# Kernel optimization log

Hardware: AMD Instinct MI355X
Metric: run time of the kernel (lower is better)

The kernel has to match this reference:

```python
import math
import jax, jax.numpy as jnp
import numpy as np

# ---- static module config ----
DIM = 256
NUM_HEADS = 8
WS = (12, 12)            # window size
L = WS[0] * WS[1]        # window area = 144
META_HIDDEN = 384
LOGIT_MAX = math.log(1.0 / 0.01)  # clamp max for logit scale


def _relative_coords_log() -> np.ndarray:
    """Log-spaced pairwise relative coordinates, shape (L*L, 2)."""
    ys, xs = np.meshgrid(np.arange(WS[0]), np.arange(WS[1]), indexing="ij")
    coords = np.stack([ys.ravel(), xs.ravel()], axis=0)          # (2, L)
    rel = coords[:, :, None] - coords[:, None, :]                # (2, L, L)
    rel = rel.transpose(1, 2, 0).reshape(-1, 2).astype(np.float32)
    return np.sign(rel) * np.log1p(np.abs(rel))

REL_COORDS_LOG = jnp.asarray(_relative_coords_log())  # (L*L, 2)


def setup_inputs() -> dict:
    key = jax.random.key(0)
    ks = jax.random.split(key, 12)
    Bw, C, H = 1024, DIM, NUM_HEADS
    num_win = 64
    inp = {
        "x": jax.random.normal(ks[0], (Bw, L, C), dtype=jnp.float32),
        "mask": jax.random.normal(ks[1], (num_win, L, L), dtype=jnp.float32),
        # qkv / proj linears
        "qkv_w": jax.random.normal(ks[2], (3 * C, C), dtype=jnp.float32) * (1.0 / math.sqrt(C)),
        "qkv_b": jnp.zeros((3 * C,), dtype=jnp.float32),
        "proj_w": jax.random.normal(ks[3], (C, C), dtype=jnp.float32) * (1.0 / math.sqrt(C)),
        "proj_b": jnp.zeros((C,), dtype=jnp.float32),
        # meta MLP: 2 -> META_HIDDEN -> H
        "fc1_w": jax.random.normal(ks[4], (META_HIDDEN, 2), dtype=jnp.float32) * 0.5,
        "fc1_b": jnp.zeros((META_HIDDEN,), dtype=jnp.float32),
        "fc2_w": jax.random.normal(ks[5], (H, META_HIDDEN), dtype=jnp.float32) * (1.0 / math.sqrt(META_HIDDEN)),
        "fc2_b": jnp.zeros((H,), dtype=jnp.float32),
        # learnable per-head logit scale, init log(10)
        "logit_scale": jnp.full((H,), math.log(10.0), dtype=jnp.float32),
    }
    return inp


def reference(x, mask, qkv_w, qkv_b, proj_w, proj_b, fc1_w, fc1_b, fc2_w, fc2_b, logit_scale):
    Bw, Lx, C = x.shape
    H = NUM_HEADS
    Dh = C // H

    # qkv projection -> (3, Bw, H, L, Dh)
    qkv = (x @ qkv_w.T + qkv_b).reshape(Bw, Lx, 3, H, Dh).transpose(2, 0, 3, 1, 4)
    q, k, v = qkv[0], qkv[1], qkv[2]

    # cosine attention: L2-normalize q and k (eps as in F.normalize)
    qn = q / jnp.maximum(jnp.linalg.norm(q, axis=-1, keepdims=True), 1e-12)
    kn = k / jnp.maximum(jnp.linalg.norm(k, axis=-1, keepdims=True), 1e-12)
    attn = jnp.einsum("bhld,bhmd->bhlm", qn, kn)  # (Bw, H, L, L)

    # clamped learnable logit scale
    scale = jnp.exp(jnp.minimum(logit_scale, LOGIT_MAX)).reshape(1, H, 1, 1)
    attn = attn * scale

    # continuous relative position bias via meta MLP (L*L, 2) -> (L*L, H)
    hbias = jax.nn.relu(REL_COORDS_LOG @ fc1_w.T + fc1_b) @ fc2_w.T + fc2_b
    rel_bias = hbias.T.reshape(1, H, Lx, Lx)
    attn = attn + rel_bias

    # shift mask: (num_win, L, L) broadcast over batch and heads
    num_win = mask.shape[0]
    attn = attn.reshape(Bw // num_win, num_win, H, Lx, Lx) + mask[None, :, None, :, :]
    attn = attn.reshape(Bw, H, Lx, Lx)

    attn = jax.nn.softmax(attn, axis=-1)

    out = jnp.einsum("bhlm,bhmd->bhld", attn, v)  # (Bw, H, L, Dh)
    out = out.transpose(0, 2, 1, 3).reshape(Bw, Lx, C)
    out = out @ proj_w.T + proj_b
    return out
```

## Files before the change

kernel.cpp:

```cpp
#include <hip/hip_runtime.h>
#include <stdint.h>


typedef __attribute__((ext_vector_type(4))) float floatx4;
typedef __attribute__((ext_vector_type(8))) __bf16 bf16x8;

#define LOGIT_MAX 4.6051701859880914f
#define LOG2E 1.4426950408889634f

__device__ __forceinline__ uint16_t f2bf(float f) {
    union { float f32; uint32_t u; } x;
    x.f32 = f;
    uint32_t r = x.u + 0x7FFFu + ((x.u >> 16) & 1u);
    return (uint16_t)(r >> 16);
}

__device__ __forceinline__ bf16x8 cvt8(const float* __restrict__ p) {
    const floatx4 a = *(const floatx4*)p;
    const floatx4 b = *(const floatx4*)(p + 4);
    union { bf16x8 v; uint16_t u[8]; } r;
    r.u[0] = f2bf(a[0]); r.u[1] = f2bf(a[1]); r.u[2] = f2bf(a[2]); r.u[3] = f2bf(a[3]);
    r.u[4] = f2bf(b[0]); r.u[5] = f2bf(b[1]); r.u[6] = f2bf(b[2]); r.u[7] = f2bf(b[3]);
    return r.v;
}

__device__ __forceinline__ void glds16(const uint16_t* g, uint16_t* l) {
    __builtin_amdgcn_global_load_lds((const __attribute__((address_space(1))) uint32_t*)g,
                                     (__attribute__((address_space(3))) uint32_t*)l, 16, 0, 0);
}

__global__ __launch_bounds__(256) void cvtw_kernel(const float* __restrict__ qkvw,
                                                   const float* __restrict__ projw,
                                                   uint16_t* __restrict__ wqkv,
                                                   uint16_t* __restrict__ wproj) {
    const int i = blockIdx.x * 256 + threadIdx.x;
    if (i < 768 * 256) wqkv[i] = f2bf(qkvw[i]);
    if (i < 256 * 256) wproj[i] = f2bf(projw[i]);
}

__global__ __launch_bounds__(256) void cvtx_kernel(const float* __restrict__ x,
                                                   uint16_t* __restrict__ xb) {
    const size_t i = (size_t)blockIdx.x * 256 + threadIdx.x;
    *(bf16x8*)(xb + i * 8) = cvt8(x + i * 8);
}

__global__ __launch_bounds__(256) void rbias_kernel(const float* __restrict__ fc1w,
                                                    const float* __restrict__ fc1b,
                                                    const float* __restrict__ fc2w,
                                                    const float* __restrict__ fc2b,
                                                    float* __restrict__ outb) {
    __shared__ float w1a[384], w1b[384], b1[384];
    __shared__ float w2[8 * 384];
    for (int i = threadIdx.x; i < 384; i += 256) {
        w1a[i] = fc1w[2 * i];
        w1b[i] = fc1w[2 * i + 1];
        b1[i]  = fc1b[i];
    }
    for (int i = threadIdx.x; i < 3072; i += 256) w2[i] = fc2w[i];
    __syncthreads();
    const int p = blockIdx.x * 256 + threadIdx.x;
    if (p >= 144 * 144) return;
    const int i = p / 144;
    const int j = p - i * 144;
    const float dy = (float)(i / 12 - j / 12);
    const float dx = (float)(i % 12 - j % 12);
    const float cy = (dy > 0.f ? 1.f : (dy < 0.f ? -1.f : 0.f)) * log1pf(fabsf(dy));
    const float cx = (dx > 0.f ? 1.f : (dx < 0.f ? -1.f : 0.f)) * log1pf(fabsf(dx));
    float acc[8] = {0, 0, 0, 0, 0, 0, 0, 0};
    for (int t = 0; t < 384; t++) {
        float hv = fmaf(cy, w1a[t], fmaf(cx, w1b[t], b1[t]));
        hv = fmaxf(hv, 0.f);
#pragma unroll
        for (int hh = 0; hh < 8; hh++) acc[hh] = fmaf(hv, w2[hh * 384 + t], acc[hh]);
    }
#pragma unroll
    for (int hh = 0; hh < 8; hh++) outb[(size_t)hh * 20736 + p] = acc[hh] + fc2b[hh];
}

__global__ __launch_bounds__(256) void gemm_qkv_kernel(const uint16_t* __restrict__ xb,
                                                       const uint16_t* __restrict__ W,
                                                       const float* __restrict__ bias,
                                                       uint16_t* __restrict__ outq) {
    __shared__ __align__(16) uint16_t sA[8192];
    __shared__ __align__(16) uint16_t sB[8192];
    const int tid  = threadIdx.x;
    const int lane = tid & 63;
    const int w    = tid >> 6;
    const int wr   = (w >> 1) << 6;
    const int wc   = (w & 1) << 6;
    const int lr   = lane & 15;
    const int q4   = lane >> 4;
    int bid = blockIdx.x;
    if ((gridDim.x & 7) == 0) {
        const int per = gridDim.x >> 3;
        bid = (bid & 7) * per + (bid >> 3);
    }
    const int brow = (bid / 6) << 7;
    const int bcol = (bid % 6) << 7;

    floatx4 acc[4][4];
#pragma unroll
    for (int m = 0; m < 4; m++)
#pragma unroll
        for (int n = 0; n < 4; n++) acc[m][n] = (floatx4){0.f, 0.f, 0.f, 0.f};

#pragma unroll 1
    for (int ks = 0; ks < 4; ++ks) {
        const int bk = ks << 6;
        __syncthreads();
#pragma unroll
        for (int i = 0; i < 4; ++i) {
            const int c = (i << 8) + tid;
            const int r = c >> 3, s = c & 7;
            const int sg = s ^ (r & 7);
            glds16(xb + (size_t)(brow + r) * 256 + bk + (sg << 3),
                   &sA[(size_t)((i << 8) + (w << 6)) << 3]);
        }
#pragma unroll
        for (int i = 0; i < 4; ++i) {
            const int c = (i << 8) + tid;
            const int r = c >> 3, s = c & 7;
            const int sg = s ^ (r & 7);
            glds16(W + (size_t)(bcol + r) * 256 + bk + (sg << 3),
                   &sB[(size_t)((i << 8) + (w << 6)) << 3]);
        }
        __syncthreads();
#pragma unroll
        for (int kk = 0; kk < 2; ++kk) {
            const int cb = (kk << 6) + (q4 << 4);
            bf16x8 af[4], bfq[4];
#pragma unroll
            for (int m = 0; m < 4; ++m) {
                const int r = wr + (m << 4) + lr;
                af[m] = *(const bf16x8*)((const char*)sA + r * 128 + (cb ^ ((r & 7) << 4)));
            }
#pragma unroll
            for (int n = 0; n < 4; ++n) {
                const int r = wc + (n << 4) + lr;
                bfq[n] = *(const bf16x8*)((const char*)sB + r * 128 + (cb ^ ((r & 7) << 4)));
            }
#pragma unroll
            for (int m = 0; m < 4; ++m)
#pragma unroll
                for (int n = 0; n < 4; ++n)
                    acc[m][n] = __builtin_amdgcn_mfma_f32_16x16x32_bf16(af[m], bfq[n], acc[m][n], 0, 0, 0);
        }
    }
#pragma unroll
    for (int n = 0; n < 4; ++n) {
        const float bb = bias[bcol + wc + (n << 4) + lr];
#pragma unroll
        for (int m = 0; m < 4; ++m)
#pragma unroll
            for (int r = 0; r < 4; ++r) acc[m][n][r] += bb;
    }
    if (bcol < 512) {
#pragma unroll
        for (int m = 0; m < 4; ++m)
#pragma unroll
            for (int np = 0; np < 4; np += 2)
#pragma unroll
                for (int r = 0; r < 4; ++r) {
                    float ss = acc[m][np][r] * acc[m][np][r] + acc[m][np + 1][r] * acc[m][np + 1][r];
#pragma unroll
                    for (int o = 1; o < 16; o <<= 1) ss += __shfl_xor(ss, o, 64);
                    const float rn = 1.0f / fmaxf(sqrtf(ss), 1e-12f);
                    acc[m][np][r] *= rn;
                    acc[m][np + 1][r] *= rn;
                }
    }
#pragma unroll
    for (int m = 0; m < 4; ++m)
#pragma unroll
        for (int r = 0; r < 4; ++r) {
            const size_t row = (size_t)(brow + wr + (m << 4) + (q4 << 2) + r);
#pragma unroll
            for (int n = 0; n < 4; ++n)
                outq[row * 768 + bcol + wc + (n << 4) + lr] = f2bf(acc[m][n][r]);
        }
}

__global__ __launch_bounds__(576, 2) void attn_kernel(const uint16_t* __restrict__ qkv,
                                                      const float* __restrict__ mask,
                                                      const float* __restrict__ rbias,
                                                      const float* __restrict__ lsc,
                                                      uint16_t* __restrict__ ob,
                                                      const int win_base, const int G) {
    __shared__ __align__(16) uint16_t sm[29568];
    uint16_t* const PB = sm;
    uint16_t* const qn = sm;
    uint16_t* const kn = sm + 5760;
    uint16_t* const vT = sm + 24192;

    int bid = blockIdx.x;
    if ((gridDim.x & 7) == 0) {
        const int per = gridDim.x >> 3;
        bid = (bid & 7) * per + (bid >> 3);
    }
    const int s4   = bid >> 3;
    const int h    = bid & 7;
    const int tid  = threadIdx.x;
    const int lane = tid & 63;
    const int mi   = tid >> 6;
    const int lr   = lane & 15;
    const int kq   = (lane >> 4) << 3;
    const int rq   = (lane >> 4) << 2;
    const int arow = mi * 16 + lr;

    const float scale2 = __expf(fminf(lsc[h], LOGIT_MAX)) * LOG2E;
    const float* bh = rbias + (size_t)h * 20736;
    const float* mw = mask + (size_t)((win_base + s4) & 63) * 20736;

    const int l   = tid >> 2;
    const int d0  = (tid & 3) << 3;
    const int rot = d0 >> 3;

    for (int i = tid; i < 32 * 24; i += 576) vT[(i / 24) * 168 + 144 + (i % 24)] = 0;

    const uint16_t* base0 = qkv + ((size_t)s4 * 144 + l) * 768 + h * 32 + d0;
    bf16x8 pq = *(const bf16x8*)(base0);
    bf16x8 pk = *(const bf16x8*)(base0 + 256);
    bf16x8 pv = *(const bf16x8*)(base0 + 512);

#pragma unroll 1
    for (int t = 0; t < G; ++t) {
        *(bf16x8*)&qn[l * 40 + d0] = pq;
        *(bf16x8*)&kn[l * 40 + d0] = pk;
        {
            union { bf16x8 v; uint16_t u[8]; } vv;
            vv.v = pv;
#pragma unroll
            for (int u = 0; u < 8; ++u) {
                const int rr = (u + rot) & 7;
                vT[(d0 + rr) * 168 + l] = vv.u[rr];
            }
        }
        __syncthreads();

        if (t + 1 < G) {
            const uint16_t* base = qkv + ((size_t)(s4 + ((t + 1) << 6)) * 144 + l) * 768 + h * 32 + d0;
            pq = *(const bf16x8*)(base);
            pk = *(const bf16x8*)(base + 256);
            pv = *(const bf16x8*)(base + 512);
        }

        const bf16x8 aq = *(const bf16x8*)&qn[arow * 40 + kq];
        float sl[9][4];
#pragma unroll
        for (int ni = 0; ni < 9; ni++) {
            const bf16x8 bkf = *(const bf16x8*)&kn[(ni * 16 + lr) * 40 + kq];
            floatx4 s = (floatx4){0.f, 0.f, 0.f, 0.f};
            s = __builtin_amdgcn_mfma_f32_16x16x32_bf16(aq, bkf, s, 0, 0, 0);
#pragma unroll
            for (int r = 0; r < 4; r++) {
                const int row = mi * 16 + rq + r;
                const int col = ni * 16 + lr;
                sl[ni][r] = fmaf(s[r], scale2, (bh[row * 144 + col] + mw[row * 144 + col]) * LOG2E);
            }
        }
#pragma unroll
        for (int r = 0; r < 4; r++) {
            float m = -3.0e38f;
#pragma unroll
            for (int ni = 0; ni < 9; ni++) m = fmaxf(m, sl[ni][r]);
#pragma unroll
            for (int o = 1; o < 16; o <<= 1) m = fmaxf(m, __shfl_xor(m, o, 64));
            float s = 0.f;
#pragma unroll
            for (int ni = 0; ni < 9; ni++) {
                float e = exp2f(sl[ni][r] - m);
                sl[ni][r] = e;
                s += e;
            }
#pragma unroll
            for (int o = 1; o < 16; o <<= 1) s += __shfl_xor(s, o, 64);
            const float inv = 1.0f / s;
#pragma unroll
            for (int ni = 0; ni < 9; ni++) sl[ni][r] *= inv;
        }
        __syncthreads();

#pragma unroll
        for (int ni = 0; ni < 9; ni++)
#pragma unroll
            for (int r = 0; r < 4; r++)
                PB[(mi * 16 + rq + r) * 168 + ni * 16 + lr] = f2bf(sl[ni][r]);
#pragma unroll
        for (int u = 0; u < 6; ++u) {
            const int idx = u * 64 + lane;
            PB[(mi * 16 + (idx / 24)) * 168 + 144 + (idx % 24)] = 0;
        }
        __syncthreads();

        floatx4 o0 = (floatx4){0.f, 0.f, 0.f, 0.f};
        floatx4 o1 = (floatx4){0.f, 0.f, 0.f, 0.f};
#pragma unroll
        for (int kt = 0; kt < 5; kt++) {
            const bf16x8 pa = *(const bf16x8*)&PB[arow * 168 + kt * 32 + kq];
            const bf16x8 v0 = *(const bf16x8*)&vT[lr * 168 + kt * 32 + kq];
            const bf16x8 v1 = *(const bf16x8*)&vT[(16 + lr) * 168 + kt * 32 + kq];
            o0 = __builtin_amdgcn_mfma_f32_16x16x32_bf16(pa, v0, o0, 0, 0, 0);
            o1 = __builtin_amdgcn_mfma_f32_16x16x32_bf16(pa, v1, o1, 0, 0, 0);
        }
#pragma unroll
        for (int r = 0; r < 4; r++) {
            const size_t row = ((size_t)s4 + ((size_t)t << 6)) * 144 + mi * 16 + rq + r;
            ob[row * 256 + h * 32 + lr]      = f2bf(o0[r]);
            ob[row * 256 + h * 32 + 16 + lr] = f2bf(o1[r]);
        }
        __syncthreads();
    }
}

__global__ __launch_bounds__(256) void gemm_proj_kernel(const uint16_t* __restrict__ A,
                                                        const uint16_t* __restrict__ W,
                                                        const float* __restrict__ bias,
                                                        float* __restrict__ outp) {
    __shared__ __align__(16) uint16_t sA[8192];
    __shared__ __align__(16) uint16_t sB[8192];
    const int tid  = threadIdx.x;
    const int lane = tid & 63;
    const int w    = tid >> 6;
    const int wr   = (w >> 1) << 6;
    const int wc   = (w & 1) << 6;
    const int lr   = lane & 15;
    const int q4   = lane >> 4;
    int bid = blockIdx.x;
    if ((gridDim.x & 7) == 0) {
        const int per = gridDim.x >> 3;
        bid = (bid & 7) * per + (bid >> 3);
    }
    const int brow = (bid >> 1) << 7;
    const int bcol = (bid & 1) << 7;

    floatx4 acc[4][4];
#pragma unroll
    for (int m = 0; m < 4; m++)
#pragma unroll
        for (int n = 0; n < 4; n++) acc[m][n] = (floatx4){0.f, 0.f, 0.f, 0.f};

#pragma unroll 1
    for (int ks = 0; ks < 4; ++ks) {
        const int bk = ks << 6;
        __syncthreads();
#pragma unroll
        for (int i = 0; i < 4; ++i) {
            const int c = (i << 8) + tid;
            const int r = c >> 3, s = c & 7;
            const int sg = s ^ (r & 7);
            glds16(A + (size_t)(brow + r) * 256 + bk + (sg << 3),
                   &sA[(size_t)((i << 8) + (w << 6)) << 3]);
        }
#pragma unroll
        for (int i = 0; i < 4; ++i) {
            const int c = (i << 8) + tid;
            const int r = c >> 3, s = c & 7;
            const int sg = s ^ (r & 7);
            glds16(W + (size_t)(bcol + r) * 256 + bk + (sg << 3),
                   &sB[(size_t)((i << 8) + (w << 6)) << 3]);
        }
        __syncthreads();
#pragma unroll
        for (int kk = 0; kk < 2; ++kk) {
            const int cb = (kk << 6) + (q4 << 4);
            bf16x8 af[4], bfq[4];
#pragma unroll
            for (int m = 0; m < 4; ++m) {
                const int r = wr + (m << 4) + lr;
                af[m] = *(const bf16x8*)((const char*)sA + r * 128 + (cb ^ ((r & 7) << 4)));
            }
#pragma unroll
            for (int n = 0; n < 4; ++n) {
                const int r = wc + (n << 4) + lr;
                bfq[n] = *(const bf16x8*)((const char*)sB + r * 128 + (cb ^ ((r & 7) << 4)));
            }
#pragma unroll
            for (int m = 0; m < 4; ++m)
#pragma unroll
                for (int n = 0; n < 4; ++n)
                    acc[m][n] = __builtin_amdgcn_mfma_f32_16x16x32_bf16(af[m], bfq[n], acc[m][n], 0, 0, 0);
        }
    }
#pragma unroll
    for (int n = 0; n < 4; ++n) {
        const float bb = bias[bcol + wc + (n << 4) + lr];
#pragma unroll
        for (int m = 0; m < 4; ++m)
#pragma unroll
            for (int r = 0; r < 4; ++r) {
                const size_t row = (size_t)(brow + wr + (m << 4) + (q4 << 2) + r);
                outp[row * 256 + bcol + wc + (n << 4) + lr] = acc[m][n][r] + bb;
            }
    }
}

extern "C" void kernel_launch(void* const* d_in, const int* in_sizes, int n_in,
                              void* d_out, int out_size, void* d_ws, size_t ws_size,
                              hipStream_t stream) {
    (void)in_sizes; (void)n_in; (void)out_size;
    const float* x      = (const float*)d_in[0];
    const float* mask   = (const float*)d_in[1];
    const float* qkv_w  = (const float*)d_in[2];
    const float* qkv_b  = (const float*)d_in[3];
    const float* proj_w = (const float*)d_in[4];
    const float* proj_b = (const float*)d_in[5];
    const float* fc1_w  = (const float*)d_in[6];
    const float* fc1_b  = (const float*)d_in[7];
    const float* fc2_w  = (const float*)d_in[8];
    const float* fc2_b  = (const float*)d_in[9];
    const float* lsc    = (const float*)d_in[10];
    float* out = (float*)d_out;

    float* bias_ws  = (float*)d_ws;
    uint16_t* wqkv  = (uint16_t*)(bias_ws + 165888);
    uint16_t* wproj = wqkv + 196608;
    uint16_t* dyn   = wproj + 65536;

    int CH = 1;
    while (CH < 128) {
        const size_t need = 1187840ULL + ((size_t)(1024 / CH) * 144) * 2560ULL;
        if (need <= ws_size) break;
        CH <<= 1;
    }
    const int WPC = 1024 / CH;
    const int MC  = WPC * 144;
    uint16_t* xbws  = dyn;
    uint16_t* qkvws = xbws + (size_t)MC * 256;
    uint16_t* obws  = qkvws + (size_t)MC * 768;

    const int S_att = (WPC >= 64) ? 64 : WPC;
    const int G     = WPC / S_att;

    cvtw_kernel<<<768, 256, 0, stream>>>(qkv_w, proj_w, wqkv, wproj);
    rbias_kernel<<<81, 256, 0, stream>>>(fc1_w, fc1_b, fc2_w, fc2_b, bias_ws);
    for (int c = 0; c < CH; ++c) {
        cvtx_kernel<<<MC / 8, 256, 0, stream>>>(x + (size_t)c * MC * 256, xbws);
        gemm_qkv_kernel<<<(MC / 128) * 6, 256, 0, stream>>>(xbws, wqkv, qkv_b, qkvws);
        attn_kernel<<<S_att * 8, 576, 0, stream>>>(qkvws, mask, bias_ws, lsc, obws,
                                                   c * WPC, G);
        gemm_proj_kernel<<<(MC / 128) * 2, 256, 0, stream>>>(obws, wproj, proj_b,
                                                             out + (size_t)c * MC * 256);
    }
}
```

Before: 704.4 us.

## Double-buffer GEMM k-tiles and precompute bias+mask in registers for attention

Measured after the change: 662.2 us. 1.06x faster.

```diff
diff --git a/kernel.cpp b/kernel.cpp
--- a/kernel.cpp
+++ b/kernel.cpp
@@ -13,6 +13,13 @@
     x.f32 = f;
     uint32_t r = x.u + 0x7FFFu + ((x.u >> 16) & 1u);
     return (uint16_t)(r >> 16);
+}
+
+__device__ __forceinline__ float bf_lo(uint32_t u) {
+    union { uint32_t v; float f; } x; x.v = u << 16; return x.f;
+}
+__device__ __forceinline__ float bf_hi(uint32_t u) {
+    union { uint32_t v; float f; } x; x.v = u & 0xffff0000u; return x.f;
 }
 
 __device__ __forceinline__ bf16x8 cvt8(const float* __restrict__ p) {
@@ -27,6 +34,22 @@
 __device__ __forceinline__ void glds16(const uint16_t* g, uint16_t* l) {
     __builtin_amdgcn_global_load_lds((const __attribute__((address_space(1))) uint32_t*)g,
                                      (__attribute__((address_space(3))) uint32_t*)l, 16, 0, 0);
+}
+
+__device__ __forceinline__ void stage2(const uint16_t* __restrict__ gA,
+                                       const uint16_t* __restrict__ gB,
+                                       uint16_t* bufA, uint16_t* bufB,
+                                       const int tid, const int w) {
+#pragma unroll
+    for (int i = 0; i < 2; ++i) {
+        const int c = (i << 8) + tid;
+        const int r = c >> 2;
+        const int sg = (c & 3) ^ ((r >> 1) & 3);
+        uint16_t* const dA = bufA + (((i << 8) + (w << 6)) << 3);
+        uint16_t* const dB = bufB + (((i << 8) + (w << 6)) << 3);
+        glds16(gA + (size_t)r * 256 + (sg << 3), dA);
+        glds16(gB + (size_t)r * 256 + (sg << 3), dB);
+    }
 }
 
 __global__ __launch_bounds__(256) void cvtw_kernel(const float* __restrict__ qkvw,
@@ -81,8 +104,8 @@
                                                        const uint16_t* __restrict__ W,
                                                        const float* __restrict__ bias,
                                                        uint16_t* __restrict__ outq) {
-    __shared__ __align__(16) uint16_t sA[8192];
-    __shared__ __align__(16) uint16_t sB[8192];
+    __shared__ __align__(16) uint16_t sA[2][4096];
+    __shared__ __align__(16) uint16_t sB[2][4096];
     const int tid  = threadIdx.x;
     const int lane = tid & 63;
     const int w    = tid >> 6;
@@ -97,6 +120,8 @@
     }
     const int brow = (bid / 6) << 7;
     const int bcol = (bid % 6) << 7;
+    const uint16_t* const gA = xb + (size_t)brow * 256;
+    const uint16_t* const gB = W + (size_t)bcol * 256;
 
     floatx4 acc[4][4];
 #pragma unroll
@@ -104,47 +129,31 @@
 #pragma unroll
         for (int n = 0; n < 4; n++) acc[m][n] = (floatx4){0.f, 0.f, 0.f, 0.f};
 
+    stage2(gA, gB, sA[0], sB[0], tid, w);
+    __syncthreads();
+    int cur = 0;
 #pragma unroll 1
-    for (int ks = 0; ks < 4; ++ks) {
-        const int bk = ks << 6;
-        __syncthreads();
-#pragma unroll
-        for (int i = 0; i < 4; ++i) {
-            const int c = (i << 8) + tid;
-            const int r = c >> 3, s = c & 7;
-            const int sg = s ^ (r & 7);
-            glds16(xb + (size_t)(brow + r) * 256 + bk + (sg << 3),
-                   &sA[(size_t)((i << 8) + (w << 6)) << 3]);
-        }
-#pragma unroll
-        for (int i = 0; i < 4; ++i) {
-            const int c = (i << 8) + tid;
-            const int r = c >> 3, s = c & 7;
-            const int sg = s ^ (r & 7);
-            glds16(W + (size_t)(bcol + r) * 256 + bk + (sg << 3),
-                   &sB[(size_t)((i << 8) + (w << 6)) << 3]);
-        }
-        __syncthreads();
-#pragma unroll
-        for (int kk = 0; kk < 2; ++kk) {
-            const int cb = (kk << 6) + (q4 << 4);
-            bf16x8 af[4], bfq[4];
-#pragma unroll
-            for (int m = 0; m < 4; ++m) {
-                const int r = wr + (m << 4) + lr;
-                af[m] = *(const bf16x8*)((const char*)sA + r * 128 + (cb ^ ((r & 7) << 4)));
-            }
-#pragma unroll
-            for (int n = 0; n < 4; ++n) {
-                const int r = wc + (n << 4) + lr;
-                bfq[n] = *(const bf16x8*)((const char*)sB + r * 128 + (cb ^ ((r & 7) << 4)));
-            }
-#pragma unroll
-            for (int m = 0; m < 4; ++m)
-#pragma unroll
-                for (int n = 0; n < 4; ++n)
-                    acc[m][n] = __builtin_amdgcn_mfma_f32_16x16x32_bf16(af[m], bfq[n], acc[m][n], 0, 0, 0);
-        }
+    for (int ks = 0; ks < 8; ++ks) {
+        if (ks < 7) stage2(gA + ((ks + 1) << 5), gB + ((ks + 1) << 5),
+                           sA[cur ^ 1], sB[cur ^ 1], tid, w);
+        bf16x8 af[4], bfq[4];
+#pragma unroll
+        for (int m = 0; m < 4; ++m) {
+            const int r = wr + (m << 4) + lr;
+            af[m] = *(const bf16x8*)((const char*)sA[cur] + r * 64 + ((q4 ^ ((r >> 1) & 3)) << 4));
+        }
+#pragma unroll
+        for (int n = 0; n < 4; ++n) {
+            const int r = wc + (n << 4) + lr;
+            bfq[n] = *(const bf16x8*)((const char*)sB[cur] + r * 64 + ((q4 ^ ((r >> 1) & 3)) << 4));
+        }
+#pragma unroll
+        for (int m = 0; m < 4; ++m)
+#pragma unroll
+            for (int n = 0; n < 4; ++n)
+                acc[m][n] = __builtin_amdgcn_mfma_f32_16x16x32_bf16(af[m], bfq[n], acc[m][n], 0, 0, 0);
+        __syncthreads();
+        cur ^= 1;
     }
 #pragma unroll
     for (int n = 0; n < 4; ++n) {
@@ -211,6 +220,18 @@
     const float* bh = rbias + (size_t)h * 20736;
     const float* mw = mask + (size_t)((win_base + s4) & 63) * 20736;
 
+    uint32_t bmp[9][2];
+#pragma unroll
+    for (int ni = 0; ni < 9; ni++)
+#pragma unroll
+        for (int rp = 0; rp < 2; rp++) {
+            const int row0 = mi * 16 + rq + rp * 2;
+            const int col  = ni * 16 + lr;
+            const float v0 = (bh[row0 * 144 + col] + mw[row0 * 144 + col]) * LOG2E;
+            const float v1 = (bh[(row0 + 1) * 144 + col] + mw[(row0 + 1) * 144 + col]) * LOG2E;
+            bmp[ni][rp] = (uint32_t)f2bf(v0) | ((uint32_t)f2bf(v1) << 16);
+        }
+
     const int l   = tid >> 2;
     const int d0  = (tid & 3) << 3;
     const int rot = d0 >> 3;
@@ -251,13 +272,12 @@
             const bf16x8 bkf = *(const bf16x8*)&kn[(ni * 16 + lr) * 40 + kq];
             floatx4 s = (floatx4){0.f, 0.f, 0.f, 0.f};
             s = __builtin_amdgcn_mfma_f32_16x16x32_bf16(aq, bkf, s, 0, 0, 0);
-#pragma unroll
-            for (int r = 0; r < 4; r++) {
-                const int row = mi * 16 + rq + r;
-                const int col = ni * 16 + lr;
-                sl[ni][r] = fmaf(s[r], scale2, (bh[row * 144 + col] + mw[row * 144 + col]) * LOG2E);
-            }
-        }
+            sl[ni][0] = fmaf(s[0], scale2, bf_lo(bmp[ni][0]));
+            sl[ni][1] = fmaf(s[1], scale2, bf_hi(bmp[ni][0]));
+            sl[ni][2] = fmaf(s[2], scale2, bf_lo(bmp[ni][1]));
+            sl[ni][3] = fmaf(s[3], scale2, bf_hi(bmp[ni][1]));
+        }
+        float invr[4];
 #pragma unroll
         for (int r = 0; r < 4; r++) {
             float m = -3.0e38f;
@@ -274,9 +294,7 @@
             }
 #pragma unroll
             for (int o = 1; o < 16; o <<= 1) s += __shfl_xor(s, o, 64);
-            const float inv = 1.0f / s;
-#pragma unroll
-            for (int ni = 0; ni < 9; ni++) sl[ni][r] *= inv;
+            invr[r] = 1.0f / s;
         }
         __syncthreads();
 
@@ -285,10 +303,12 @@
 #pragma unroll
             for (int r = 0; r < 4; r++)
                 PB[(mi * 16 + rq + r) * 168 + ni * 16 + lr] = f2bf(sl[ni][r]);
-#pragma unroll
-        for (int u = 0; u < 6; ++u) {
-            const int idx = u * 64 + lane;
-            PB[(mi * 16 + (idx / 24)) * 168 + 144 + (idx % 24)] = 0;
+        if (t == 0 || mi <= 4) {
+#pragma unroll
+            for (int u = 0; u < 6; ++u) {
+                const int idx = u * 64 + lane;
+                PB[(mi * 16 + (idx / 24)) * 168 + 144 + (idx % 24)] = 0;
+            }
         }
         __syncthreads();
 
@@ -305,8 +325,8 @@
 #pragma unroll
         for (int r = 0; r < 4; r++) {
             const size_t row = ((size_t)s4 + ((size_t)t << 6)) * 144 + mi * 16 + rq + r;
-            ob[row * 256 + h * 32 + lr]      = f2bf(o0[r]);
-            ob[row * 256 + h * 32 + 16 + lr] = f2bf(o1[r]);
+            ob[row * 256 + h * 32 + lr]      = f2bf(o0[r] * invr[r]);
+            ob[row * 256 + h * 32 + 16 + lr] = f2bf(o1[r] * invr[r]);
         }
         __syncthreads();
     }
@@ -316,8 +336,8 @@
                                                         const uint16_t* __restrict__ W,
                                                         const float* __restrict__ bias,
                                                         float* __restrict__ outp) {
-    __shared__ __align__(16) uint16_t sA[8192];
-    __shared__ __align__(16) uint16_t sB[8192];
+    __shared__ __align__(16) uint16_t sA[2][4096];
+    __shared__ __align__(16) uint16_t sB[2][4096];
     const int tid  = threadIdx.x;
     const int lane = tid & 63;
     const int w    = tid >> 6;
@@ -332,6 +352,8 @@
     }
     const int brow = (bid >> 1) << 7;
     const int bcol = (bid & 1) << 7;
+    const uint16_t* const gA = A + (size_t)brow * 256;
+    const uint16_t* const gB = W + (size_t)bcol * 256;
 
     floatx4 acc[4][4];
 #pragma unroll
@@ -339,47 +361,31 @@
 #pragma unroll
         for (int n = 0; n < 4; n++) acc[m][n] = (floatx4){0.f, 0.f, 0.f, 0.f};
 
+    stage2(gA, gB, sA[0], sB[0], tid, w);
+    __syncthreads();
+    int cur = 0;
 #pragma unroll 1
-    for (int ks = 0; ks < 4; ++ks) {
-        const int bk = ks << 6;
-        __syncthreads();
-#pragma unroll
-        for (int i = 0; i < 4; ++i) {
-            const int c = (i << 8) + tid;
-            const int r = c >> 3, s = c & 7;
-            const int sg = s ^ (r & 7);
-            glds16(A + (size_t)(brow + r) * 256 + bk + (sg << 3),
-                   &sA[(size_t)((i << 8) + (w << 6)) << 3]);
-        }
-#pragma unroll
-        for (int i = 0; i < 4; ++i) {
-            const int c = (i << 8) + tid;
-            const int r = c >> 3, s = c & 7;
-            const int sg = s ^ (r & 7);
-            glds16(W + (size_t)(bcol + r) * 256 + bk + (sg << 3),
-                   &sB[(size_t)((i << 8) + (w << 6)) << 3]);
-        }
-        __syncthreads();
-#pragma unroll
-        for (int kk = 0; kk < 2; ++kk) {
-            const int cb = (kk << 6) + (q4 << 4);
-            bf16x8 af[4], bfq[4];
-#pragma unroll
-            for (int m = 0; m < 4; ++m) {
-                const int r = wr + (m << 4) + lr;
-                af[m] = *(const bf16x8*)((const char*)sA + r * 128 + (cb ^ ((r & 7) << 4)));
-            }
-#pragma unroll
-            for (int n = 0; n < 4; ++n) {
-                const int r = wc + (n << 4) + lr;
-                bfq[n] = *(const bf16x8*)((const char*)sB + r * 128 + (cb ^ ((r & 7) << 4)));
-            }
-#pragma unroll
-            for (int m = 0; m < 4; ++m)
-#pragma unroll
-                for (int n = 0; n < 4; ++n)
-                    acc[m][n] = __builtin_amdgcn_mfma_f32_16x16x32_bf16(af[m], bfq[n], acc[m][n], 0, 0, 0);
-        }
+    for (int ks = 0; ks < 8; ++ks) {
+        if (ks < 7) stage2(gA + ((ks + 1) << 5), gB + ((ks + 1) << 5),
+                           sA[cur ^ 1], sB[cur ^ 1], tid, w);
+        bf16x8 af[4], bfq[4];
+#pragma unroll
+        for (int m = 0; m < 4; ++m) {
+            const int r = wr + (m << 4) + lr;
+            af[m] = *(const bf16x8*)((const char*)sA[cur] + r * 64 + ((q4 ^ ((r >> 1) & 3)) << 4));
+        }
+#pragma unroll
+        for (int n = 0; n < 4; ++n) {
+            const int r = wc + (n << 4) + lr;
+            bfq[n] = *(const bf16x8*)((const char*)sB[cur] + r * 64 + ((q4 ^ ((r >> 1) & 3)) << 4));
+        }
+#pragma unroll
+        for (int m = 0; m < 4; ++m)
+#pragma unroll
+            for (int n = 0; n < 4; ++n)
+                acc[m][n] = __builtin_amdgcn_mfma_f32_16x16x32_bf16(af[m], bfq[n], acc[m][n], 0, 0, 0);
+        __syncthreads();
+        cur ^= 1;
     }
 #pragma unroll
     for (int n = 0; n < 4; ++n) {
```
